# Kernel tuning notes

Measured on AMD Instinct MI355X. Metric: run time of the kernel, lower is better.

## Reference

```python
import jax, jax.numpy as jnp
import numpy as np

B, L, D = 4, 4096, 2048
DF = 4 * D
CAPACITY_RATIO = 0.5


def setup_inputs() -> dict:
    key = jax.random.key(0)
    ks = jax.random.split(key, 4)
    s = 0.02
    return {
        "x": jax.random.normal(ks[0], (B, L, D), dtype=jnp.float32),
        "w_r": jax.random.normal(ks[1], (D,), dtype=jnp.float32) * s,
        "b_r": jnp.zeros((), dtype=jnp.float32),
        "w1": jax.random.normal(ks[2], (D, DF), dtype=jnp.float32) * s,
        "b1": jnp.zeros((DF,), dtype=jnp.float32),
        "w2": jax.random.normal(ks[3], (DF, D), dtype=jnp.float32) * s,
        "b2": jnp.zeros((D,), dtype=jnp.float32),
    }


def reference(x, w_r, b_r, w1, b1, w2, b2):
    # MoD eval path: router scores -> top-k token indices -> gather ->
    # block (FFN) on selected tokens -> scatter back into zeros.
    b, l, d = x.shape
    k = int(l * CAPACITY_RATIO)
    scores = jnp.einsum("bld,d->bl", x, w_r) + b_r          # [B, L]
    _, idx = jax.lax.top_k(scores, k)                        # [B, k] int32
    x_sel = jnp.take_along_axis(x, idx[:, :, None], axis=1)  # [B, k, D]
    h = jax.nn.gelu(jnp.einsum("bkd,df->bkf", x_sel, w1) + b1)
    out_sel = jnp.einsum("bkf,fd->bkd", h, w2) + b2          # [B, k, D]
    batch_ix = jnp.arange(b)[:, None]                        # [B, 1]
    out = jnp.zeros_like(x).at[batch_ix, idx].set(out_sel)
    return out
```

## Files before the change

kernel.cpp:

```cpp
#include <hip/hip_runtime.h>

#define BB 4
#define LL 4096
#define DD 2048
#define DFF 8192
#define KSEL 2048
#define MROWS (BB * KSEL)

typedef __bf16 bf16x8 __attribute__((ext_vector_type(8)));
typedef float f32x4 __attribute__((ext_vector_type(4)));
typedef unsigned short u16x8 __attribute__((ext_vector_type(8)));

__device__ __forceinline__ unsigned short f2bf(float f) {
    union { float f; unsigned int u; } v; v.f = f;
    unsigned int u = v.u;
    unsigned int r = u + 0x7fffu + ((u >> 16) & 1u);
    return (unsigned short)(r >> 16);
}

__device__ __forceinline__ void gl2lds16(const void* g, void* l) {
    __builtin_amdgcn_global_load_lds(
        (const __attribute__((address_space(1))) void*)g,
        (__attribute__((address_space(3))) void*)l,
        16, 0, 0);
}

__global__ __launch_bounds__(256) void router_kernel(
    const float* __restrict__ x, const float* __restrict__ wr,
    const float* __restrict__ br, float* __restrict__ scores)
{
    const int lane = threadIdx.x & 63;
    const int wave = threadIdx.x >> 6;
    const int tok = blockIdx.x * 4 + wave;
    const float* row = x + (long)tok * DD;
    double acc = 0.0;
#pragma unroll
    for (int it = 0; it < 8; ++it) {
        const int off = it * 256 + lane * 4;
        float4 xv = *(const float4*)(row + off);
        float4 wv = *(const float4*)(wr + off);
        acc += (double)xv.x * wv.x + (double)xv.y * wv.y
             + (double)xv.z * wv.z + (double)xv.w * wv.w;
    }
#pragma unroll
    for (int o = 32; o > 0; o >>= 1) acc += __shfl_down(acc, o);
    if (lane == 0) scores[tok] = (float)(acc + (double)br[0]);
}

__global__ __launch_bounds__(256) void rank_select_kernel(
    const float* __restrict__ scores, int* __restrict__ idxout)
{
    __shared__ float s[LL];
    const int b = blockIdx.y;
    const float* sb = scores + b * LL;
    for (int i = threadIdx.x; i < LL; i += 256) s[i] = sb[i];
    __syncthreads();
    const int t = blockIdx.x * 256 + threadIdx.x;
    const float my = s[t];
    int rank = 0;
#pragma unroll 16
    for (int j = 0; j < LL; ++j) {
        float sj = s[j];
        rank += (sj > my) || (sj == my && j < t);
    }
    if (rank < KSEL) idxout[(b << 11) + rank] = t;
}

__global__ __launch_bounds__(256) void conv_transpose_kernel(
    const float* __restrict__ W, unsigned short* __restrict__ Wt,
    int KR, int NC)
{
    __shared__ unsigned short t[64 * 72];
    const int n0 = blockIdx.x * 64;
    const int k0 = blockIdx.y * 64;
    const int tid = threadIdx.x;
    const int rk = tid >> 4;
    const int cn = (tid & 15) * 4;
#pragma unroll
    for (int p = 0; p < 4; ++p) {
        const int k = rk + p * 16;
        float4 v = *(const float4*)(W + (long)(k0 + k) * NC + n0 + cn);
        t[(cn + 0) * 72 + k] = f2bf(v.x);
        t[(cn + 1) * 72 + k] = f2bf(v.y);
        t[(cn + 2) * 72 + k] = f2bf(v.z);
        t[(cn + 3) * 72 + k] = f2bf(v.w);
    }
    __syncthreads();
    const int rn = tid >> 3;
    const int ck = (tid & 7) * 8;
#pragma unroll
    for (int p = 0; p < 2; ++p) {
        const int n = rn + p * 32;
        u16x8 o = *(const u16x8*)&t[n * 72 + ck];
        *(u16x8*)(Wt + (long)(n0 + n) * KR + k0 + ck) = o;
    }
}

__global__ __launch_bounds__(256) void gather_rows_kernel(
    const float* __restrict__ x, const int* __restrict__ idx,
    unsigned short* __restrict__ xsel)
{
    const int m = blockIdx.x;
    const int b = m >> 11;
    const int tok = idx[m];
    const float* src = x + ((long)b * LL + tok) * DD;
    unsigned short* dst = xsel + (long)m * DD;
    const int c = threadIdx.x * 8;
    float4 v0 = *(const float4*)(src + c);
    float4 v1 = *(const float4*)(src + c + 4);
    u16x8 o;
    o[0] = f2bf(v0.x); o[1] = f2bf(v0.y); o[2] = f2bf(v0.z); o[3] = f2bf(v0.w);
    o[4] = f2bf(v1.x); o[5] = f2bf(v1.y); o[6] = f2bf(v1.z); o[7] = f2bf(v1.w);
    *(u16x8*)(dst + c) = o;
}

template <int MODE>
__global__ __launch_bounds__(256, 3) void gemm_bt_kernel(
    const unsigned short* __restrict__ A,
    const unsigned short* __restrict__ Bt,
    const float* __restrict__ bias,
    unsigned short* __restrict__ H,
    const int* __restrict__ idx,
    float* __restrict__ Out,
    int K, int N)
{
    __shared__ unsigned short As[2 * 128 * 32];
    __shared__ unsigned short Bs[2 * 128 * 32];
    const int tid = threadIdx.x;
    const int lane = tid & 63;
    const int wave = tid >> 6;
    const int wm = wave >> 1, wn = wave & 1;

    const int npn = gridDim.x;
    const int pid = blockIdx.y * npn + blockIdx.x;
    const int per_grp = 32 * npn;
    const int gid = pid / per_grp;
    const int rem = pid - gid * per_grp;
    const int pm = gid * 32 + (rem & 31);
    const int pn = rem >> 5;
    const long m0 = (long)pm * 128;
    const long n0 = (long)pn * 128;

    const int c0 = wave * 128 + lane;
    const int c1 = c0 + 64;
    const unsigned short* gA0 = A + (m0 + (c0 >> 2)) * K + (c0 & 3) * 8;
    const unsigned short* gA1 = A + (m0 + (c1 >> 2)) * K + (c1 & 3) * 8;
    const unsigned short* gB0 = Bt + (n0 + (c0 >> 2)) * K + (c0 & 3) * 8;
    const unsigned short* gB1 = Bt + (n0 + (c1 >> 2)) * K + (c1 & 3) * 8;
    unsigned short* lA0 = As + wave * 1024;
    unsigned short* lA1 = As + wave * 1024 + 512;
    unsigned short* lB0 = Bs + wave * 1024;
    unsigned short* lB1 = Bs + wave * 1024 + 512;

    f32x4 acc[4][4];
#pragma unroll
    for (int i = 0; i < 4; ++i)
#pragma unroll
        for (int j = 0; j < 4; ++j) {
            f32x4 z = {0.f, 0.f, 0.f, 0.f};
            acc[i][j] = z;
        }

    const int arow = wm * 64 + (lane & 15);
    const int brow = wn * 64 + (lane & 15);
    const int qk = (lane >> 4) * 8;

    for (int kt = 0; kt < K; kt += 64) {
#pragma unroll
        for (int h = 0; h < 2; ++h) {
            gl2lds16(gA0 + kt + 32 * h, lA0 + h * 4096);
            gl2lds16(gA1 + kt + 32 * h, lA1 + h * 4096);
            gl2lds16(gB0 + kt + 32 * h, lB0 + h * 4096);
            gl2lds16(gB1 + kt + 32 * h, lB1 + h * 4096);
        }
        __syncthreads();
#pragma unroll
        for (int s = 0; s < 2; ++s) {
            const unsigned short* as = As + s * 4096;
            const unsigned short* bs = Bs + s * 4096;
            bf16x8 af[4], bfm[4];
#pragma unroll
            for (int i = 0; i < 4; ++i)
                af[i] = *(const bf16x8*)&as[(arow + i * 16) * 32 + qk];
#pragma unroll
            for (int j = 0; j < 4; ++j)
                bfm[j] = *(const bf16x8*)&bs[(brow + j * 16) * 32 + qk];
#pragma unroll
            for (int i = 0; i < 4; ++i)
#pragma unroll
                for (int j = 0; j < 4; ++j)
                    acc[i][j] = __builtin_amdgcn_mfma_f32_16x16x32_bf16(
                        af[i], bfm[j], acc[i][j], 0, 0, 0);
        }
        __syncthreads();
    }

    const int colbase = (int)n0 + wn * 64 + (lane & 15);
    const long rowbase = m0 + wm * 64 + ((lane >> 4) << 2);

    if constexpr (MODE == 0) {
#pragma unroll
        for (int i = 0; i < 4; ++i) {
#pragma unroll
            for (int j = 0; j < 4; ++j) {
                const int col = colbase + j * 16;
                const float bv = bias[col];
#pragma unroll
                for (int r = 0; r < 4; ++r) {
                    const long row = rowbase + i * 16 + r;
                    float v = acc[i][j][r] + bv;
                    float u = v + 0.044715f * v * v * v;
                    float e = __expf(1.5957691216057308f * u);
                    float g = v - v * __builtin_amdgcn_rcpf(1.0f + e);
                    H[row * N + col] = f2bf(g);
                }
            }
        }
    } else {
        long obase[4][4];
#pragma unroll
        for (int i = 0; i < 4; ++i)
#pragma unroll
            for (int r = 0; r < 4; ++r) {
                const int row = (int)(rowbase + i * 16 + r);
                const int b = row >> 11;
                const int rr = row & (KSEL - 1);
                const int tok = idx[(b << 11) + rr];
                obase[i][r] = ((long)(b * LL + tok)) * DD;
            }
#pragma unroll
        for (int j = 0; j < 4; ++j) {
            const int col = colbase + j * 16;
            const float bv = bias[col];
#pragma unroll
            for (int i = 0; i < 4; ++i)
#pragma unroll
                for (int r = 0; r < 4; ++r)
                    Out[obase[i][r] + col] = acc[i][j][r] + bv;
        }
    }
}

extern "C" void kernel_launch(void* const* d_in, const int* in_sizes, int n_in,
                              void* d_out, int out_size, void* d_ws, size_t ws_size,
                              hipStream_t stream)
{
    const float* x  = (const float*)d_in[0];
    const float* wr = (const float*)d_in[1];
    const float* br = (const float*)d_in[2];
    const float* w1 = (const float*)d_in[3];
    const float* b1 = (const float*)d_in[4];
    const float* w2 = (const float*)d_in[5];
    const float* b2 = (const float*)d_in[6];
    float* out = (float*)d_out;

    char* ws = (char*)d_ws;
    float* scores = (float*)ws;              ws += (long)BB * LL * 4;
    int* idx = (int*)ws;                     ws += (long)BB * KSEL * 4;
    unsigned short* xsel = (unsigned short*)ws; ws += (long)MROWS * DD * 2;
    unsigned short* w1t  = (unsigned short*)ws; ws += (long)DFF * DD * 2;
    unsigned short* w2t  = (unsigned short*)ws; ws += (long)DD * DFF * 2;
    unsigned short* h    = (unsigned short*)ws; ws += (long)MROWS * DFF * 2;

    hipMemsetAsync(d_out, 0, (size_t)out_size * sizeof(float), stream);

    router_kernel<<<(BB * LL) / 4, 256, 0, stream>>>(x, wr, br, scores);
    rank_select_kernel<<<dim3(LL / 256, BB), 256, 0, stream>>>(scores, idx);
    conv_transpose_kernel<<<dim3(DFF / 64, DD / 64), 256, 0, stream>>>(
        w1, w1t, DD, DFF);
    conv_transpose_kernel<<<dim3(DD / 64, DFF / 64), 256, 0, stream>>>(
        w2, w2t, DFF, DD);
    gather_rows_kernel<<<MROWS, 256, 0, stream>>>(x, idx, xsel);
    gemm_bt_kernel<0><<<dim3(DFF / 128, MROWS / 128), 256, 0, stream>>>(
        xsel, w1t, b1, h, nullptr, nullptr, DD, DFF);
    gemm_bt_kernel<1><<<dim3(DD / 128, MROWS / 128), 256, 0, stream>>>(
        h, w2t, b2, nullptr, idx, out, DFF, DD);
}
```

Before: 1.056 ms.

## Fuse bf16 conversion into router, gather in GEMM, zero only unselected rows

```diff
diff --git a/kernel.cpp b/kernel.cpp
--- a/kernel.cpp
+++ b/kernel.cpp
@@ -25,22 +25,32 @@
         16, 0, 0);
 }
 
-__global__ __launch_bounds__(256) void router_kernel(
+__global__ __launch_bounds__(256) void router_conv_kernel(
     const float* __restrict__ x, const float* __restrict__ wr,
-    const float* __restrict__ br, float* __restrict__ scores)
+    const float* __restrict__ br, float* __restrict__ scores,
+    unsigned short* __restrict__ xbf)
 {
     const int lane = threadIdx.x & 63;
     const int wave = threadIdx.x >> 6;
     const int tok = blockIdx.x * 4 + wave;
     const float* row = x + (long)tok * DD;
+    unsigned short* orow = xbf + (long)tok * DD;
     double acc = 0.0;
 #pragma unroll
-    for (int it = 0; it < 8; ++it) {
-        const int off = it * 256 + lane * 4;
+    for (int it = 0; it < 4; ++it) {
+        const int off = it * 512 + lane * 8;
         float4 xv = *(const float4*)(row + off);
+        float4 xw = *(const float4*)(row + off + 4);
         float4 wv = *(const float4*)(wr + off);
+        float4 ww = *(const float4*)(wr + off + 4);
         acc += (double)xv.x * wv.x + (double)xv.y * wv.y
              + (double)xv.z * wv.z + (double)xv.w * wv.w;
+        acc += (double)xw.x * ww.x + (double)xw.y * ww.y
+             + (double)xw.z * ww.z + (double)xw.w * ww.w;
+        u16x8 o;
+        o[0] = f2bf(xv.x); o[1] = f2bf(xv.y); o[2] = f2bf(xv.z); o[3] = f2bf(xv.w);
+        o[4] = f2bf(xw.x); o[5] = f2bf(xw.y); o[6] = f2bf(xw.z); o[7] = f2bf(xw.w);
+        *(u16x8*)(orow + off) = o;
     }
 #pragma unroll
     for (int o = 32; o > 0; o >>= 1) acc += __shfl_down(acc, o);
@@ -48,7 +58,8 @@
 }
 
 __global__ __launch_bounds__(256) void rank_select_kernel(
-    const float* __restrict__ scores, int* __restrict__ idxout)
+    const float* __restrict__ scores, int* __restrict__ idxout,
+    int* __restrict__ zidxout)
 {
     __shared__ float s[LL];
     const int b = blockIdx.y;
@@ -64,15 +75,33 @@
         rank += (sj > my) || (sj == my && j < t);
     }
     if (rank < KSEL) idxout[(b << 11) + rank] = t;
-}
-
-__global__ __launch_bounds__(256) void conv_transpose_kernel(
-    const float* __restrict__ W, unsigned short* __restrict__ Wt,
-    int KR, int NC)
+    else             zidxout[(b << 11) + rank - KSEL] = t;
+}
+
+__global__ __launch_bounds__(256) void zero_rows_kernel(
+    const int* __restrict__ zidx, float* __restrict__ Out)
+{
+    const int m = blockIdx.x;
+    const int b = m >> 11;
+    const int tok = zidx[m];
+    float* dst = Out + ((long)b * LL + tok) * DD;
+    const int c = threadIdx.x * 8;
+    float4 z = {0.f, 0.f, 0.f, 0.f};
+    *(float4*)(dst + c) = z;
+    *(float4*)(dst + c + 4) = z;
+}
+
+__global__ __launch_bounds__(256) void conv_transpose2_kernel(
+    const float* __restrict__ W1, unsigned short* __restrict__ W1t,
+    const float* __restrict__ W2, unsigned short* __restrict__ W2t)
 {
     __shared__ unsigned short t[64 * 72];
-    const int n0 = blockIdx.x * 64;
-    const int k0 = blockIdx.y * 64;
+    int bid = blockIdx.x;
+    const float* W; unsigned short* Wt; int KR, NC, bx, by;
+    if (bid < 4096) { W = W1; Wt = W1t; KR = DD; NC = DFF; bx = bid & 127; by = bid >> 7; }
+    else { bid -= 4096; W = W2; Wt = W2t; KR = DFF; NC = DD; bx = bid & 31; by = bid >> 5; }
+    const int n0 = bx * 64;
+    const int k0 = by * 64;
     const int tid = threadIdx.x;
     const int rk = tid >> 4;
     const int cn = (tid & 15) * 4;
@@ -96,26 +125,8 @@
     }
 }
 
-__global__ __launch_bounds__(256) void gather_rows_kernel(
-    const float* __restrict__ x, const int* __restrict__ idx,
-    unsigned short* __restrict__ xsel)
-{
-    const int m = blockIdx.x;
-    const int b = m >> 11;
-    const int tok = idx[m];
-    const float* src = x + ((long)b * LL + tok) * DD;
-    unsigned short* dst = xsel + (long)m * DD;
-    const int c = threadIdx.x * 8;
-    float4 v0 = *(const float4*)(src + c);
-    float4 v1 = *(const float4*)(src + c + 4);
-    u16x8 o;
-    o[0] = f2bf(v0.x); o[1] = f2bf(v0.y); o[2] = f2bf(v0.z); o[3] = f2bf(v0.w);
-    o[4] = f2bf(v1.x); o[5] = f2bf(v1.y); o[6] = f2bf(v1.z); o[7] = f2bf(v1.w);
-    *(u16x8*)(dst + c) = o;
-}
-
-template <int MODE>
-__global__ __launch_bounds__(256, 3) void gemm_bt_kernel(
+template <int MODE, int IND>
+__global__ __launch_bounds__(256, 4) void gemm_bt_kernel(
     const unsigned short* __restrict__ A,
     const unsigned short* __restrict__ Bt,
     const float* __restrict__ bias,
@@ -143,8 +154,17 @@
 
     const int c0 = wave * 128 + lane;
     const int c1 = c0 + 64;
-    const unsigned short* gA0 = A + (m0 + (c0 >> 2)) * K + (c0 & 3) * 8;
-    const unsigned short* gA1 = A + (m0 + (c1 >> 2)) * K + (c1 & 3) * 8;
+    long ar0, ar1;
+    if constexpr (IND) {
+        const int r0 = (int)m0 + (c0 >> 2), r1 = (int)m0 + (c1 >> 2);
+        ar0 = (long)(r0 >> 11) * LL + idx[r0];
+        ar1 = (long)(r1 >> 11) * LL + idx[r1];
+    } else {
+        ar0 = m0 + (c0 >> 2);
+        ar1 = m0 + (c1 >> 2);
+    }
+    const unsigned short* gA0 = A + ar0 * K + (c0 & 3) * 8;
+    const unsigned short* gA1 = A + ar1 * K + (c1 & 3) * 8;
     const unsigned short* gB0 = Bt + (n0 + (c0 >> 2)) * K + (c0 & 3) * 8;
     const unsigned short* gB1 = Bt + (n0 + (c1 >> 2)) * K + (c1 & 3) * 8;
     unsigned short* lA0 = As + wave * 1024;
@@ -256,23 +276,19 @@
 
     char* ws = (char*)d_ws;
     float* scores = (float*)ws;              ws += (long)BB * LL * 4;
-    int* idx = (int*)ws;                     ws += (long)BB * KSEL * 4;
-    unsigned short* xsel = (unsigned short*)ws; ws += (long)MROWS * DD * 2;
+    int* idx  = (int*)ws;                    ws += (long)BB * KSEL * 4;
+    int* zidx = (int*)ws;                    ws += (long)BB * (LL - KSEL) * 4;
+    unsigned short* xbf  = (unsigned short*)ws; ws += (long)BB * LL * DD * 2;
     unsigned short* w1t  = (unsigned short*)ws; ws += (long)DFF * DD * 2;
     unsigned short* w2t  = (unsigned short*)ws; ws += (long)DD * DFF * 2;
     unsigned short* h    = (unsigned short*)ws; ws += (long)MROWS * DFF * 2;
 
-    hipMemsetAsync(d_out, 0, (size_t)out_size * sizeof(float), stream);
-
-    router_kernel<<<(BB * LL) / 4, 256, 0, stream>>>(x, wr, br, scores);
-    rank_select_kernel<<<dim3(LL / 256, BB), 256, 0, stream>>>(scores, idx);
-    conv_transpose_kernel<<<dim3(DFF / 64, DD / 64), 256, 0, stream>>>(
-        w1, w1t, DD, DFF);
-    conv_transpose_kernel<<<dim3(DD / 64, DFF / 64), 256, 0, stream>>>(
-        w2, w2t, DFF, DD);
-    gather_rows_kernel<<<MROWS, 256, 0, stream>>>(x, idx, xsel);
-    gemm_bt_kernel<0><<<dim3(DFF / 128, MROWS / 128), 256, 0, stream>>>(
-        xsel, w1t, b1, h, nullptr, nullptr, DD, DFF);
-    gemm_bt_kernel<1><<<dim3(DD / 128, MROWS / 128), 256, 0, stream>>>(
+    router_conv_kernel<<<(BB * LL) / 4, 256, 0, stream>>>(x, wr, br, scores, xbf);
+    conv_transpose2_kernel<<<8192, 256, 0, stream>>>(w1, w1t, w2, w2t);
+    rank_select_kernel<<<dim3(LL / 256, BB), 256, 0, stream>>>(scores, idx, zidx);
+    zero_rows_kernel<<<BB * (LL - KSEL), 256, 0, stream>>>(zidx, out);
+    gemm_bt_kernel<0, 1><<<dim3(DFF / 128, MROWS / 128), 256, 0, stream>>>(
+        xbf, w1t, b1, h, idx, nullptr, DD, DFF);
+    gemm_bt_kernel<1, 0><<<dim3(DD / 128, MROWS / 128), 256, 0, stream>>>(
         h, w2t, b2, nullptr, idx, out, DFF, DD);
 }
```

New measurement: 1.054 ms. Within noise of the previous version (-0.1%).
